# Performance work log

Measured on AMD Instinct MI355X. Metric: run time of the kernel, lower is better.

The kernel has to match this reference:

```python
import jax, jax.numpy as jnp
import numpy as np

N_NODES = 50000
N_EDGES = 800000
D_FEAT = 64
EDGE_DIM = 64


def setup_inputs() -> dict:
    key = jax.random.key(0)
    k1, k2, k3, k4 = jax.random.split(key, 4)
    node_feats = jax.random.normal(k1, (N_NODES, D_FEAT), dtype=jnp.float32)
    senders = jax.random.randint(k2, (N_EDGES,), 0, N_NODES, dtype=jnp.int32)
    receivers = jax.random.randint(k3, (N_EDGES,), 0, N_NODES, dtype=jnp.int32)
    # Dense(edge_dim) applied to concat([recv, send]) of width 2*D_FEAT
    W = jax.random.normal(k4, (2 * D_FEAT, EDGE_DIM), dtype=jnp.float32) / np.sqrt(2.0 * D_FEAT)
    b = jnp.zeros((EDGE_DIM,), dtype=jnp.float32)
    return {"node_feats": node_feats, "senders": senders, "receivers": receivers, "W": W, "b": b}


def reference(node_feats, senders, receivers, W, b):
    # gather node features at each edge endpoint: [E, D]
    feats_send = node_feats[senders]
    feats_recv = node_feats[receivers]
    # concat(recv, send) -> [E, 2D], Dense + tanh -> [E, edge_dim]
    edge_feats = jnp.concatenate([feats_recv, feats_send], axis=-1)
    return jnp.tanh(edge_feats @ W + b)
```

## Files before the change

### kernel.cpp

```cpp
#include <hip/hip_runtime.h>

#define N_EDGES 800000
#define N_NODES 50000
#define D 64
#define WT_STRIDE 136

typedef __attribute__((ext_vector_type(8))) short bf16x8;
typedef __attribute__((ext_vector_type(4))) float f32x4;

__device__ __forceinline__ unsigned short f2bf(float f) {
    unsigned int u = __float_as_uint(f);
    u += 0x7fffu + ((u >> 16) & 1u);
    return (unsigned short)(u >> 16);
}
__device__ __forceinline__ unsigned int pack2(float a, float b) {
    return (unsigned int)f2bf(a) | ((unsigned int)f2bf(b) << 16);
}

__global__ __launch_bounds__(256) void prep(
    const float* __restrict__ nf, const float* __restrict__ W,
    unsigned short* __restrict__ nodes_bf, unsigned short* __restrict__ wt_bf)
{
    if (blockIdx.x == gridDim.x - 1) {
        for (int i = threadIdx.x; i < D * 128; i += 256) {
            const int n = i >> 7, k = i & 127;
            wt_bf[n * WT_STRIDE + k] = f2bf(W[k * D + n]);
        }
    } else {
        const long base = ((long)blockIdx.x * 256 + threadIdx.x) * 8;
        if (base < (long)N_NODES * D) {
            const float4 lo = *(const float4*)(nf + base);
            const float4 hi = *(const float4*)(nf + base + 4);
            uint4 p;
            p.x = pack2(lo.x, lo.y);
            p.y = pack2(lo.z, lo.w);
            p.z = pack2(hi.x, hi.y);
            p.w = pack2(hi.z, hi.w);
            *(uint4*)(nodes_bf + base) = p;
        }
    }
}

__global__ __launch_bounds__(256) void edge_mlp(
    const unsigned short* __restrict__ nodes_bf,
    const unsigned short* __restrict__ wt_bf,
    const int*   __restrict__ senders,
    const int*   __restrict__ receivers,
    const float* __restrict__ bias,
    float*       __restrict__ out)
{
    const int lane = threadIdx.x & 63;
    const int m    = lane & 15;
    const int q    = lane >> 4;
    const long wid = (long)blockIdx.x * 4 + (threadIdx.x >> 6);
    const long e0  = wid * 64;
    if (e0 >= N_EDGES) return;

    int nidx[2][4];
#pragma unroll
    for (int mt = 0; mt < 4; ++mt) {
        const long e = e0 + mt * 16 + m;
        nidx[0][mt] = receivers[e];
        nidx[1][mt] = senders[e];
    }

    f32x4 acc[4][4];
#pragma unroll
    for (int mt = 0; mt < 4; ++mt)
#pragma unroll
        for (int nt = 0; nt < 4; ++nt)
            acc[mt][nt] = (f32x4)0.0f;

#pragma unroll
    for (int ki = 0; ki < 4; ++ki) {
        const int k0 = ki * 32 + q * 8;

        bf16x8 bfrag[4];
#pragma unroll
        for (int nt = 0; nt < 4; ++nt)
            bfrag[nt] = *(const bf16x8*)(wt_bf + (nt * 16 + m) * WT_STRIDE + k0);

        bf16x8 afrag[4];
#pragma unroll
        for (int mt = 0; mt < 4; ++mt) {
            const int node = nidx[ki >> 1][mt];
            afrag[mt] = *(const bf16x8*)(nodes_bf + node * D + (k0 & 63));
        }

#pragma unroll
        for (int mt = 0; mt < 4; ++mt)
#pragma unroll
            for (int nt = 0; nt < 4; ++nt)
                acc[mt][nt] = __builtin_amdgcn_mfma_f32_16x16x32_bf16(
                    afrag[mt], bfrag[nt], acc[mt][nt], 0, 0, 0);
    }

    float bv[4];
#pragma unroll
    for (int nt = 0; nt < 4; ++nt) bv[nt] = bias[nt * 16 + m];

#pragma unroll
    for (int mt = 0; mt < 4; ++mt) {
#pragma unroll
        for (int r = 0; r < 4; ++r) {
            const long row = e0 + mt * 16 + q * 4 + r;
            float* op = out + row * D + m;
#pragma unroll
            for (int nt = 0; nt < 4; ++nt) {
                const float x  = acc[mt][nt][r] + bv[nt];
                const float ax = __builtin_fabsf(x);
                const float t  = __expf(-2.0f * ax);
                float y = (1.0f - t) * __builtin_amdgcn_rcpf(1.0f + t);
                y = __builtin_copysignf(y, x);
                __builtin_nontemporal_store(y, op + nt * 16);
            }
        }
    }
}

extern "C" void kernel_launch(void* const* d_in, const int* in_sizes, int n_in,
                              void* d_out, int out_size, void* d_ws, size_t ws_size,
                              hipStream_t stream) {
    const float* node_feats = (const float*)d_in[0];
    const int*   senders    = (const int*)d_in[1];
    const int*   receivers  = (const int*)d_in[2];
    const float* W          = (const float*)d_in[3];
    const float* bias       = (const float*)d_in[4];
    float*       out        = (float*)d_out;

    unsigned short* nodes_bf = (unsigned short*)d_ws;
    unsigned short* wt_bf    = (unsigned short*)((char*)d_ws + (size_t)N_NODES * D * 2);

    const int node_blocks = ((N_NODES * D / 8) + 255) / 256;
    prep<<<node_blocks + 1, 256, 0, stream>>>(node_feats, W, nodes_bf, wt_bf);

    const int n_blocks = (N_EDGES + 255) / 256;
    edge_mlp<<<n_blocks, 256, 0, stream>>>(nodes_bf, wt_bf, senders, receivers, bias, out);
}
```

Baseline: 274.3 us.

## Pre-swizzle weight fragments, stage them in LDS, and shuffle edge indices

The prep kernel now writes the bf16 weights already arranged in MFMA B-fragment order. Each edge block copies those fragments into shared memory once and reads the B operands from LDS, replacing per-wave strided global loads. Edge indices are loaded once per lane with coalesced reads and spread to the fragment rows with wavefront shuffles, instead of four separate loads each. The bounds check is removed and the grid assumes N_EDGES divides by 256 exactly. Each block now pays an extra 16KB LDS fill and a barrier.

```diff
diff --git a/kernel.cpp b/kernel.cpp
--- a/kernel.cpp
+++ b/kernel.cpp
@@ -3,7 +3,6 @@
 #define N_EDGES 800000
 #define N_NODES 50000
 #define D 64
-#define WT_STRIDE 136
 
 typedef __attribute__((ext_vector_type(8))) short bf16x8;
 typedef __attribute__((ext_vector_type(4))) float f32x4;
@@ -19,12 +18,22 @@
 
 __global__ __launch_bounds__(256) void prep(
     const float* __restrict__ nf, const float* __restrict__ W,
-    unsigned short* __restrict__ nodes_bf, unsigned short* __restrict__ wt_bf)
+    unsigned short* __restrict__ nodes_bf, unsigned short* __restrict__ wfrag)
 {
     if (blockIdx.x == gridDim.x - 1) {
-        for (int i = threadIdx.x; i < D * 128; i += 256) {
-            const int n = i >> 7, k = i & 127;
-            wt_bf[n * WT_STRIDE + k] = f2bf(W[k * D + n]);
+#pragma unroll
+        for (int i = 0; i < 4; ++i) {
+            const int idx = i * 256 + threadIdx.x;
+            const int ki = idx >> 8;
+            const int nt = (idx >> 6) & 3;
+            const int l  = idx & 63;
+            const int m  = l & 15, q = l >> 4;
+            const int kbase = ki * 32 + q * 8;
+            const int n = nt * 16 + m;
+            unsigned short* dst = wfrag + idx * 8;
+#pragma unroll
+            for (int j = 0; j < 8; ++j)
+                dst[j] = f2bf(W[(kbase + j) * D + n]);
         }
     } else {
         const long base = ((long)blockIdx.x * 256 + threadIdx.x) * 8;
@@ -43,25 +52,34 @@
 
 __global__ __launch_bounds__(256) void edge_mlp(
     const unsigned short* __restrict__ nodes_bf,
-    const unsigned short* __restrict__ wt_bf,
+    const bf16x8*        __restrict__ wfrag,
     const int*   __restrict__ senders,
     const int*   __restrict__ receivers,
     const float* __restrict__ bias,
     float*       __restrict__ out)
 {
+    __shared__ bf16x8 lds_b[1024];
+
+#pragma unroll
+    for (int i = 0; i < 4; ++i) {
+        const int idx = i * 256 + threadIdx.x;
+        lds_b[idx] = wfrag[idx];
+    }
+    __syncthreads();
+
     const int lane = threadIdx.x & 63;
     const int m    = lane & 15;
     const int q    = lane >> 4;
     const long wid = (long)blockIdx.x * 4 + (threadIdx.x >> 6);
     const long e0  = wid * 64;
-    if (e0 >= N_EDGES) return;
 
+    const int rv = receivers[e0 + lane];
+    const int sv = senders[e0 + lane];
     int nidx[2][4];
 #pragma unroll
     for (int mt = 0; mt < 4; ++mt) {
-        const long e = e0 + mt * 16 + m;
-        nidx[0][mt] = receivers[e];
-        nidx[1][mt] = senders[e];
+        nidx[0][mt] = __shfl(rv, mt * 16 + m, 64);
+        nidx[1][mt] = __shfl(sv, mt * 16 + m, 64);
     }
 
     f32x4 acc[4][4];
@@ -78,7 +96,7 @@
         bf16x8 bfrag[4];
 #pragma unroll
         for (int nt = 0; nt < 4; ++nt)
-            bfrag[nt] = *(const bf16x8*)(wt_bf + (nt * 16 + m) * WT_STRIDE + k0);
+            bfrag[nt] = lds_b[(ki * 4 + nt) * 64 + lane];
 
         bf16x8 afrag[4];
 #pragma unroll
@@ -129,11 +147,12 @@
     float*       out        = (float*)d_out;
 
     unsigned short* nodes_bf = (unsigned short*)d_ws;
-    unsigned short* wt_bf    = (unsigned short*)((char*)d_ws + (size_t)N_NODES * D * 2);
+    unsigned short* wfrag    = (unsigned short*)((char*)d_ws + (size_t)N_NODES * D * 2);
 
     const int node_blocks = ((N_NODES * D / 8) + 255) / 256;
-    prep<<<node_blocks + 1, 256, 0, stream>>>(node_feats, W, nodes_bf, wt_bf);
+    prep<<<node_blocks + 1, 256, 0, stream>>>(node_feats, W, nodes_bf, wfrag);
 
-    const int n_blocks = (N_EDGES + 255) / 256;
-    edge_mlp<<<n_blocks, 256, 0, stream>>>(nodes_bf, wt_bf, senders, receivers, bias, out);
+    const int n_blocks = N_EDGES / 256;
+    edge_mlp<<<n_blocks, 256, 0, stream>>>(nodes_bf, (const bf16x8*)wfrag,
+                                           senders, receivers, bias, out);
 }
```

Result: faster. 257.2 us (-6.2%).
